# Kernel tuning notes

Hardware: AMD Instinct MI355X
Metric: run time of the kernel (lower is better)

## Reference

```python
import jax, jax.numpy as jnp
import numpy as np

H = 16          # num_heads
WIN = 256       # window_size

def setup_inputs() -> dict:
    key = jax.random.key(0)
    k1, k2, k3, k4 = jax.random.split(key, 4)
    B, N, C = 2, 4096, 1024
    x = jax.random.normal(k1, (B, N, C), dtype=jnp.float32)
    w_qkv = jax.random.normal(k2, (C, 3 * C), dtype=jnp.float32) * 0.02
    w_proj = jax.random.normal(k3, (C, C), dtype=jnp.float32) * 0.02
    b_proj = jax.random.normal(k4, (C,), dtype=jnp.float32) * 0.02
    return {"x": x, "w_qkv": w_qkv, "w_proj": w_proj, "b_proj": b_proj}

def reference(x, w_qkv, w_proj, b_proj):
    B, N, C = x.shape
    D = C // H
    scale = D ** -0.5
    b = WIN // 2            # block size = half window radius; window = [i-b, i+b]
    nb = N // b             # number of query blocks (N divisible by b here)

    qkv = (x @ w_qkv).reshape(B, N, 3, H, D).transpose(2, 0, 3, 1, 4)  # [3,B,H,N,D]
    q, k, v = qkv[0], qkv[1], qkv[2]                                   # [B,H,N,D]

    qb = q.reshape(B, H, nb, b, D)                                     # [B,H,nb,b,D]
    # pad keys/values by one block on each side, gather 3-block windows
    kp = jnp.pad(k, ((0, 0), (0, 0), (b, b), (0, 0)))                  # [B,H,N+2b,D]
    vp = jnp.pad(v, ((0, 0), (0, 0), (b, b), (0, 0)))
    win_idx = jnp.arange(nb)[:, None] * b + jnp.arange(3 * b)[None, :]  # [nb,3b]
    kw = kp[:, :, win_idx]                                             # [B,H,nb,3b,D]
    vw = vp[:, :, win_idx]

    scores = jnp.einsum('bhnqd,bhnkd->bhnqk', qb, kw) * scale          # [B,H,nb,b,3b]

    # mask: key global pos = j*b + ki - b ; query global pos = j*b + qi
    qi = jnp.arange(b)[:, None]           # [b,1]
    ki = jnp.arange(3 * b)[None, :]       # [1,3b]
    rel_ok = jnp.abs(ki - b - qi) <= b    # [b,3b]  |key - query| <= W/2
    key_pos = (jnp.arange(nb)[:, None] * b + jnp.arange(3 * b)[None, :]) - b  # [nb,3b]
    in_range = (key_pos >= 0) & (key_pos < N)                          # [nb,3b]
    valid = rel_ok[None, :, :] & in_range[:, None, :]                  # [nb,b,3b]

    scores = jnp.where(valid[None, None], scores, -jnp.inf)
    attn = jax.nn.softmax(scores, axis=-1)
    out = jnp.einsum('bhnqk,bhnkd->bhnqd', attn, vw)                   # [B,H,nb,b,D]
    out = out.reshape(B, H, N, D).transpose(0, 2, 1, 3).reshape(B, N, C)
    return out @ w_proj + b_proj
```

## Files before the change

kernel.cpp:

```cpp
#include <hip/hip_runtime.h>

typedef unsigned short ushort_t;
typedef __attribute__((ext_vector_type(8))) short short8;
typedef __attribute__((ext_vector_type(8))) unsigned short ushort8;
typedef __attribute__((ext_vector_type(4))) unsigned short us4;
typedef __attribute__((ext_vector_type(4))) float f32x4;

__device__ __forceinline__ ushort_t f2bf(float f) {
  union { float f; unsigned int u; } x; x.f = f;
  unsigned int r = x.u + 0x7fffu + ((x.u >> 16) & 1u);
  return (ushort_t)(r >> 16);
}

__device__ __forceinline__ void async16(const void* g, void* lds_uniform) {
  __builtin_amdgcn_global_load_lds(
      (const __attribute__((address_space(1))) void*)g,
      (__attribute__((address_space(3))) void*)lds_uniform, 16, 0, 0);
}

__global__ __launch_bounds__(256) void prep_fused(
    const float* __restrict__ x, ushort_t* __restrict__ x16,
    const float* __restrict__ w_qkv, ushort_t* __restrict__ wqkvT,
    const float* __restrict__ w_proj, ushort_t* __restrict__ wprojT)
{
  __shared__ float tile[32][33];
  const int bid = blockIdx.x;
  const int tid = threadIdx.x;
  if (bid < 1024) {
    for (int i = bid * 256 + tid; i < 2097152; i += 1024 * 256) {
      float4 f = ((const float4*)x)[i];
      us4 u;
      u[0] = f2bf(f.x); u[1] = f2bf(f.y); u[2] = f2bf(f.z); u[3] = f2bf(f.w);
      ((us4*)x16)[i] = u;
    }
  } else {
    const float* in; ushort_t* out; int Cc, bx, by;
    if (bid < 4096) {
      in = w_qkv; out = wqkvT; Cc = 3072;
      bx = ((bid - 1024) % 96) * 32; by = ((bid - 1024) / 96) * 32;
    } else {
      in = w_proj; out = wprojT; Cc = 1024;
      bx = ((bid - 4096) & 31) * 32; by = ((bid - 4096) >> 5) * 32;
    }
    const int tx = tid & 31, ty = tid >> 5;
    #pragma unroll
    for (int i = ty; i < 32; i += 8)
      tile[i][tx] = in[(size_t)(by + i) * Cc + bx + tx];
    __syncthreads();
    #pragma unroll
    for (int i = ty; i < 32; i += 8)
      out[(size_t)(bx + i) * 1024 + by + tx] = f2bf(tile[tx][i]);
  }
}

template<int MODE>
__global__ __launch_bounds__(256) void gemm128(
    const ushort_t* __restrict__ A, const ushort_t* __restrict__ Bt,
    ushort_t* __restrict__ o0, ushort_t* __restrict__ o1, ushort_t* __restrict__ o2,
    const float* __restrict__ bias, float* __restrict__ fout)
{
  constexpr int K = 1024;
  __shared__ __align__(16) ushort_t As[128 * 64];
  __shared__ __align__(16) ushort_t Bs[128 * 64];
  const int tm = blockIdx.y * 128;
  const int tn = blockIdx.x * 128;
  const int tid = threadIdx.x;
  const int w = tid >> 6, lane = tid & 63;
  const int wr = (w >> 1) * 64, wc = (w & 1) * 64;
  const int l15 = lane & 15, lq = lane >> 4;

  const int srow = lane >> 3;
  const int scol = ((lane & 7) ^ srow) << 3;

  const int offk0 = (lq ^ (l15 & 7)) << 4;
  const int offk1 = ((4 + lq) ^ (l15 & 7)) << 4;
  const char* aRd = (const char*)As + (size_t)(wr + l15) * 128;
  const char* bRd = (const char*)Bs + (size_t)(wc + l15) * 128;

  f32x4 acc[4][4] = {};

  for (int k0 = 0; k0 < K; k0 += 64) {
    #pragma unroll
    for (int j = 0; j < 4; ++j) {
      const int c = w * 4 + j;
      const int row = c * 8 + srow;
      async16(A  + (size_t)(tm + row) * K + k0 + scol, (char*)As + c * 1024);
      async16(Bt + (size_t)(tn + row) * K + k0 + scol, (char*)Bs + c * 1024);
    }
    __syncthreads();
    #pragma unroll
    for (int kk = 0; kk < 2; ++kk) {
      const int offk = kk ? offk1 : offk0;
      short8 af[4], bfr[4];
      #pragma unroll
      for (int i = 0; i < 4; ++i) {
        af[i]  = *(const short8*)(aRd + i * 2048 + offk);
        bfr[i] = *(const short8*)(bRd + i * 2048 + offk);
      }
      #pragma unroll
      for (int i = 0; i < 4; ++i)
        #pragma unroll
        for (int j = 0; j < 4; ++j)
          acc[i][j] = __builtin_amdgcn_mfma_f32_16x16x32_bf16(af[i], bfr[j], acc[i][j], 0, 0, 0);
    }
    __syncthreads();
  }

  if (MODE == 0) {
    #pragma unroll
    for (int j = 0; j < 4; ++j) {
      const int col = tn + wc + j * 16 + l15;
      const int which = col >> 10;
      const int h = (col >> 6) & 15, d = col & 63;
      ushort_t* dst = (which == 0) ? o0 : ((which == 1) ? o1 : o2);
      #pragma unroll
      for (int i = 0; i < 4; ++i)
        #pragma unroll
        for (int r = 0; r < 4; ++r) {
          const int m = tm + wr + i * 16 + lq * 4 + r;
          const int b = m >> 12, n = m & 4095;
          dst[(size_t)((b * 16 + h) * 4096 + n) * 64 + d] = f2bf(acc[i][j][r]);
        }
    }
  } else {
    #pragma unroll
    for (int j = 0; j < 4; ++j) {
      const int col = tn + wc + j * 16 + l15;
      const float bv = bias[col];
      #pragma unroll
      for (int i = 0; i < 4; ++i)
        #pragma unroll
        for (int r = 0; r < 4; ++r) {
          const int m = tm + wr + i * 16 + lq * 4 + r;
          fout[(size_t)m * 1024 + col] = acc[i][j][r] + bv;
        }
    }
  }
}

__global__ __launch_bounds__(256) void swin_attn(
    const ushort_t* __restrict__ qb, const ushort_t* __restrict__ kb,
    const ushort_t* __restrict__ vb, ushort_t* __restrict__ attn_out)
{
  constexpr int N = 4096;
  __shared__ __align__(16) ushort_t Ks[64 * 64];
  __shared__ __align__(16) ushort_t VT[64 * 72];
  __shared__ __align__(16) ushort_t Pw[4][32 * 72];
  const int qblk = blockIdx.x;
  const int bh = blockIdx.y;
  const int tid = threadIdx.x;
  const int w = tid >> 6, lane = tid & 63;
  const int l15 = lane & 15, lq = lane >> 4;
  const size_t base = (size_t)bh * N * 64;
  const int q0 = qblk * 128 + w * 32;

  const int offk0 = (lq ^ (l15 & 7)) << 4;
  const int offk1 = ((4 + lq) ^ (l15 & 7)) << 4;
  const int srow = lane >> 3;
  const int scol = ((lane & 7) ^ srow) << 3;

  short8 qf[2][2];
  #pragma unroll
  for (int fm = 0; fm < 2; ++fm)
    #pragma unroll
    for (int kk = 0; kk < 2; ++kk)
      qf[fm][kk] = *(const short8*)&qb[base + (size_t)(q0 + fm * 16 + l15) * 64 + kk * 32 + lq * 8];

  const short ones_bf = (short)0x3F80;
  const short8 ones8 = short8{ones_bf, ones_bf, ones_bf, ones_bf,
                              ones_bf, ones_bf, ones_bf, ones_bf};

  f32x4 oacc[2][5] = {};

  for (int t = 0; t < 6; ++t) {
    const int kpos0 = qblk * 128 - 128 + t * 64;
    if (kpos0 + 63 < 0 || kpos0 >= N) continue;
    const bool active = (kpos0 <= q0 + 31 + 128) && (kpos0 + 63 >= q0 - 128);
    __syncthreads();
    #pragma unroll
    for (int j = 0; j < 2; ++j) {
      const int c = w * 2 + j;
      const int row = c * 8 + srow;
      int kp = kpos0 + row; kp = kp < 0 ? 0 : (kp > N - 1 ? N - 1 : kp);
      async16(kb + base + (size_t)kp * 64 + scol, (char*)Ks + c * 1024);
    }
    {
      const int key = tid >> 2;
      const int dbase = (tid & 3) * 16;
      int kp = kpos0 + key; kp = kp < 0 ? 0 : (kp > N - 1 ? N - 1 : kp);
      const ushort_t* src = vb + base + (size_t)kp * 64 + dbase;
      ushort8 v0 = *(const ushort8*)src;
      ushort8 v1 = *(const ushort8*)(src + 8);
      #pragma unroll
      for (int i = 0; i < 8; ++i) VT[(dbase + i) * 72 + key] = v0[i];
      #pragma unroll
      for (int i = 0; i < 8; ++i) VT[(dbase + 8 + i) * 72 + key] = v1[i];
    }
    __syncthreads();
    if (!active) continue;

    f32x4 sacc[2][4] = {};
    #pragma unroll
    for (int kk = 0; kk < 2; ++kk) {
      const int offk = kk ? offk1 : offk0;
      short8 kf[4];
      #pragma unroll
      for (int fn = 0; fn < 4; ++fn)
        kf[fn] = *(const short8*)((const char*)Ks + (fn * 16 + l15) * 128 + offk);
      #pragma unroll
      for (int fm = 0; fm < 2; ++fm)
        #pragma unroll
        for (int fn = 0; fn < 4; ++fn)
          sacc[fm][fn] = __builtin_amdgcn_mfma_f32_16x16x32_bf16(qf[fm][kk], kf[fn], sacc[fm][fn], 0, 0, 0);
    }

    int kposl[4]; bool inr[4];
    #pragma unroll
    for (int fn = 0; fn < 4; ++fn) {
      kposl[fn] = kpos0 + fn * 16 + l15;
      inr[fn] = (kposl[fn] >= 0) && (kposl[fn] < N);
    }
    #pragma unroll
    for (int fm = 0; fm < 2; ++fm) {
      #pragma unroll
      for (int r = 0; r < 4; ++r) {
        const int qpos = q0 + fm * 16 + lq * 4 + r;
        #pragma unroll
        for (int fn = 0; fn < 4; ++fn) {
          const int dd = kposl[fn] - qpos;
          const bool valid = inr[fn] && (dd <= 128) && (dd >= -128);
          const float p = valid ? __expf(sacc[fm][fn][r] * 0.125f) : 0.f;
          Pw[w][(fm * 16 + lq * 4 + r) * 72 + fn * 16 + l15] = f2bf(p);
        }
      }
    }

    #pragma unroll
    for (int kk = 0; kk < 2; ++kk) {
      short8 pf[2], vf[4];
      #pragma unroll
      for (int fm = 0; fm < 2; ++fm)
        pf[fm] = *(const short8*)&Pw[w][(fm * 16 + l15) * 72 + kk * 32 + lq * 8];
      #pragma unroll
      for (int fn = 0; fn < 4; ++fn)
        vf[fn] = *(const short8*)&VT[(fn * 16 + l15) * 72 + kk * 32 + lq * 8];
      #pragma unroll
      for (int fm = 0; fm < 2; ++fm) {
        #pragma unroll
        for (int fn = 0; fn < 4; ++fn)
          oacc[fm][fn] = __builtin_amdgcn_mfma_f32_16x16x32_bf16(pf[fm], vf[fn], oacc[fm][fn], 0, 0, 0);
        oacc[fm][4] = __builtin_amdgcn_mfma_f32_16x16x32_bf16(pf[fm], ones8, oacc[fm][4], 0, 0, 0);
      }
    }
  }

  const int b = bh >> 4, h = bh & 15;
  #pragma unroll
  for (int fm = 0; fm < 2; ++fm)
    #pragma unroll
    for (int r = 0; r < 4; ++r) {
      const float inv = 1.0f / oacc[fm][4][r];
      const int qpos = q0 + fm * 16 + lq * 4 + r;
      #pragma unroll
      for (int fn = 0; fn < 4; ++fn) {
        const int d = fn * 16 + l15;
        attn_out[(size_t)(b * 4096 + qpos) * 1024 + h * 64 + d] = f2bf(oacc[fm][fn][r] * inv);
      }
    }
}

extern "C" void kernel_launch(void* const* d_in, const int* in_sizes, int n_in,
                              void* d_out, int out_size, void* d_ws, size_t ws_size,
                              hipStream_t stream) {
  const float* x      = (const float*)d_in[0];
  const float* w_qkv  = (const float*)d_in[1];
  const float* w_proj = (const float*)d_in[2];
  const float* b_proj = (const float*)d_in[3];
  float* out = (float*)d_out;
  char* ws = (char*)d_ws;

  ushort_t* x16    = (ushort_t*)(ws);
  ushort_t* wqkvT  = (ushort_t*)(ws + 16777216);
  ushort_t* wprojT = (ushort_t*)(ws + 23068672);
  ushort_t* qbuf   = (ushort_t*)(ws + 25165824);
  ushort_t* kbuf   = (ushort_t*)(ws + 41943040);
  ushort_t* vbuf   = (ushort_t*)(ws + 58720256);
  ushort_t* attn16 = x16;

  prep_fused<<<dim3(5120), dim3(256), 0, stream>>>(x, x16, w_qkv, wqkvT, w_proj, wprojT);
  gemm128<0><<<dim3(24, 64), dim3(256), 0, stream>>>(x16, wqkvT, qbuf, kbuf, vbuf, nullptr, nullptr);
  swin_attn<<<dim3(32, 32), dim3(256), 0, stream>>>(qbuf, kbuf, vbuf, attn16);
  gemm128<1><<<dim3(8, 64), dim3(256), 0, stream>>>(attn16, wprojT, nullptr, nullptr, nullptr, b_proj, out);
}
```

Measured before the change: 136.8 us.

## Double-buffer K/V tiles in windowed attention to overlap loads with MFMA compute

The windowed attention kernel now keeps two LDS buffers for K and transposed V. It prefetches the next 64-key tile (async K copy, register-staged V) while computing on the current one, and needs only one barrier per iteration instead of two. Loop bounds are computed up front so out-of-range tiles at the sequence edges are skipped, which removes the clamping and in-range mask checks. The cost is double the K/V LDS footprint and extra registers for the staged V data, which may lower occupancy.

```diff
diff --git a/kernel.cpp b/kernel.cpp
--- a/kernel.cpp
+++ b/kernel.cpp
@@ -143,8 +143,8 @@
     const ushort_t* __restrict__ vb, ushort_t* __restrict__ attn_out)
 {
   constexpr int N = 4096;
-  __shared__ __align__(16) ushort_t Ks[64 * 64];
-  __shared__ __align__(16) ushort_t VT[64 * 72];
+  __shared__ __align__(16) ushort_t Ks2[2][64 * 64];
+  __shared__ __align__(16) ushort_t VT2[2][64 * 72];
   __shared__ __align__(16) ushort_t Pw[4][32 * 72];
   const int qblk = blockIdx.x;
   const int bh = blockIdx.y;
@@ -159,6 +159,12 @@
   const int srow = lane >> 3;
   const int scol = ((lane & 7) ^ srow) << 3;
 
+  const int vkey = tid >> 2;
+  const int vdbase = (tid & 3) * 16;
+
+  const int t_lo = (qblk == 0) ? 2 : 0;
+  const int t_hi = (qblk == 31) ? 3 : 5;
+
   short8 qf[2][2];
   #pragma unroll
   for (int fm = 0; fm < 2; ++fm)
@@ -172,86 +178,103 @@
 
   f32x4 oacc[2][5] = {};
 
-  for (int t = 0; t < 6; ++t) {
-    const int kpos0 = qblk * 128 - 128 + t * 64;
-    if (kpos0 + 63 < 0 || kpos0 >= N) continue;
-    const bool active = (kpos0 <= q0 + 31 + 128) && (kpos0 + 63 >= q0 - 128);
-    __syncthreads();
+  {
+    const int kpos0 = qblk * 128 - 128 + t_lo * 64;
     #pragma unroll
     for (int j = 0; j < 2; ++j) {
       const int c = w * 2 + j;
       const int row = c * 8 + srow;
-      int kp = kpos0 + row; kp = kp < 0 ? 0 : (kp > N - 1 ? N - 1 : kp);
-      async16(kb + base + (size_t)kp * 64 + scol, (char*)Ks + c * 1024);
-    }
-    {
-      const int key = tid >> 2;
-      const int dbase = (tid & 3) * 16;
-      int kp = kpos0 + key; kp = kp < 0 ? 0 : (kp > N - 1 ? N - 1 : kp);
-      const ushort_t* src = vb + base + (size_t)kp * 64 + dbase;
-      ushort8 v0 = *(const ushort8*)src;
-      ushort8 v1 = *(const ushort8*)(src + 8);
-      #pragma unroll
-      for (int i = 0; i < 8; ++i) VT[(dbase + i) * 72 + key] = v0[i];
-      #pragma unroll
-      for (int i = 0; i < 8; ++i) VT[(dbase + 8 + i) * 72 + key] = v1[i];
+      async16(kb + base + (size_t)(kpos0 + row) * 64 + scol, (char*)Ks2[0] + c * 1024);
+    }
+    const ushort_t* src = vb + base + (size_t)(kpos0 + vkey) * 64 + vdbase;
+    ushort8 v0 = *(const ushort8*)src;
+    ushort8 v1 = *(const ushort8*)(src + 8);
+    #pragma unroll
+    for (int i = 0; i < 8; ++i) VT2[0][(vdbase + i) * 72 + vkey] = v0[i];
+    #pragma unroll
+    for (int i = 0; i < 8; ++i) VT2[0][(vdbase + 8 + i) * 72 + vkey] = v1[i];
+  }
+  __syncthreads();
+
+  int c = 0;
+  for (int t = t_lo; t <= t_hi; ++t) {
+    const int kpos0 = qblk * 128 - 128 + t * 64;
+    const bool has_next = (t < t_hi);
+    ushort8 nv0, nv1;
+    if (has_next) {
+      const int knext = kpos0 + 64;
+      #pragma unroll
+      for (int j = 0; j < 2; ++j) {
+        const int cc = w * 2 + j;
+        const int row = cc * 8 + srow;
+        async16(kb + base + (size_t)(knext + row) * 64 + scol, (char*)Ks2[c ^ 1] + cc * 1024);
+      }
+      const ushort_t* src = vb + base + (size_t)(knext + vkey) * 64 + vdbase;
+      nv0 = *(const ushort8*)src;
+      nv1 = *(const ushort8*)(src + 8);
+    }
+
+    const bool active = (kpos0 <= q0 + 31 + 128) && (kpos0 + 63 >= q0 - 128);
+    if (active) {
+      const ushort_t* Ks = Ks2[c];
+      const ushort_t* VT = VT2[c];
+      f32x4 sacc[2][4] = {};
+      #pragma unroll
+      for (int kk = 0; kk < 2; ++kk) {
+        const int offk = kk ? offk1 : offk0;
+        short8 kf[4];
+        #pragma unroll
+        for (int fn = 0; fn < 4; ++fn)
+          kf[fn] = *(const short8*)((const char*)Ks + (fn * 16 + l15) * 128 + offk);
+        #pragma unroll
+        for (int fm = 0; fm < 2; ++fm)
+          #pragma unroll
+          for (int fn = 0; fn < 4; ++fn)
+            sacc[fm][fn] = __builtin_amdgcn_mfma_f32_16x16x32_bf16(qf[fm][kk], kf[fn], sacc[fm][fn], 0, 0, 0);
+      }
+
+      #pragma unroll
+      for (int fm = 0; fm < 2; ++fm) {
+        #pragma unroll
+        for (int r = 0; r < 4; ++r) {
+          const int qpos = q0 + fm * 16 + lq * 4 + r;
+          #pragma unroll
+          for (int fn = 0; fn < 4; ++fn) {
+            const int dd = kpos0 + fn * 16 + l15 - qpos;
+            const bool valid = (dd <= 128) && (dd >= -128);
+            const float p = valid ? __expf(sacc[fm][fn][r] * 0.125f) : 0.f;
+            Pw[w][(fm * 16 + lq * 4 + r) * 72 + fn * 16 + l15] = f2bf(p);
+          }
+        }
+      }
+
+      #pragma unroll
+      for (int kk = 0; kk < 2; ++kk) {
+        short8 pf[2], vf[4];
+        #pragma unroll
+        for (int fm = 0; fm < 2; ++fm)
+          pf[fm] = *(const short8*)&Pw[w][(fm * 16 + l15) * 72 + kk * 32 + lq * 8];
+        #pragma unroll
+        for (int fn = 0; fn < 4; ++fn)
+          vf[fn] = *(const short8*)&VT[(fn * 16 + l15) * 72 + kk * 32 + lq * 8];
+        #pragma unroll
+        for (int fm = 0; fm < 2; ++fm) {
+          #pragma unroll
+          for (int fn = 0; fn < 4; ++fn)
+            oacc[fm][fn] = __builtin_amdgcn_mfma_f32_16x16x32_bf16(pf[fm], vf[fn], oacc[fm][fn], 0, 0, 0);
+          oacc[fm][4] = __builtin_amdgcn_mfma_f32_16x16x32_bf16(pf[fm], ones8, oacc[fm][4], 0, 0, 0);
+        }
+      }
+    }
+
+    if (has_next) {
+      #pragma unroll
+      for (int i = 0; i < 8; ++i) VT2[c ^ 1][(vdbase + i) * 72 + vkey] = nv0[i];
+      #pragma unroll
+      for (int i = 0; i < 8; ++i) VT2[c ^ 1][(vdbase + 8 + i) * 72 + vkey] = nv1[i];
     }
     __syncthreads();
-    if (!active) continue;
-
-    f32x4 sacc[2][4] = {};
-    #pragma unroll
-    for (int kk = 0; kk < 2; ++kk) {
-      const int offk = kk ? offk1 : offk0;
-      short8 kf[4];
-      #pragma unroll
-      for (int fn = 0; fn < 4; ++fn)
-        kf[fn] = *(const short8*)((const char*)Ks + (fn * 16 + l15) * 128 + offk);
-      #pragma unroll
-      for (int fm = 0; fm < 2; ++fm)
-        #pragma unroll
-        for (int fn = 0; fn < 4; ++fn)
-          sacc[fm][fn] = __builtin_amdgcn_mfma_f32_16x16x32_bf16(qf[fm][kk], kf[fn], sacc[fm][fn], 0, 0, 0);
-    }
-
-    int kposl[4]; bool inr[4];
-    #pragma unroll
-    for (int fn = 0; fn < 4; ++fn) {
-      kposl[fn] = kpos0 + fn * 16 + l15;
-      inr[fn] = (kposl[fn] >= 0) && (kposl[fn] < N);
-    }
-    #pragma unroll
-    for (int fm = 0; fm < 2; ++fm) {
-      #pragma unroll
-      for (int r = 0; r < 4; ++r) {
-        const int qpos = q0 + fm * 16 + lq * 4 + r;
-        #pragma unroll
-        for (int fn = 0; fn < 4; ++fn) {
-          const int dd = kposl[fn] - qpos;
-          const bool valid = inr[fn] && (dd <= 128) && (dd >= -128);
-          const float p = valid ? __expf(sacc[fm][fn][r] * 0.125f) : 0.f;
-          Pw[w][(fm * 16 + lq * 4 + r) * 72 + fn * 16 + l15] = f2bf(p);
-        }
-      }
-    }
-
-    #pragma unroll
-    for (int kk = 0; kk < 2; ++kk) {
-      short8 pf[2], vf[4];
-      #pragma unroll
-      for (int fm = 0; fm < 2; ++fm)
-        pf[fm] = *(const short8*)&Pw[w][(fm * 16 + l15) * 72 + kk * 32 + lq * 8];
-      #pragma unroll
-      for (int fn = 0; fn < 4; ++fn)
-        vf[fn] = *(const short8*)&VT[(fn * 16 + l15) * 72 + kk * 32 + lq * 8];
-      #pragma unroll
-      for (int fm = 0; fm < 2; ++fm) {
-        #pragma unroll
-        for (int fn = 0; fn < 4; ++fn)
-          oacc[fm][fn] = __builtin_amdgcn_mfma_f32_16x16x32_bf16(pf[fm], vf[fn], oacc[fm][fn], 0, 0, 0);
-        oacc[fm][4] = __builtin_amdgcn_mfma_f32_16x16x32_bf16(pf[fm], ones8, oacc[fm][4], 0, 0, 0);
-      }
-    }
+    c ^= 1;
   }
 
   const int b = bh >> 4, h = bh & 15;
```

Result: no change. 135.4 us (-1.0%).
